# Optimization experiments

Hardware: AMD Instinct MI355X
Metric: run time of the kernel (lower is better)

The kernel has to match this reference:

```python
import jax, jax.numpy as jnp
import numpy as np

H = 64            # hidden_dim
N_NODES = 100000
N_EDGES = 2000000
IN_DIM = 2 * H + 2  # src_emb || dst_emb || src_fiedler || dst_fiedler


def setup_inputs() -> dict:
    key = jax.random.key(0)
    ks = jax.random.split(key, 10)
    node_embeddings = jax.random.normal(ks[0], (N_NODES, H), dtype=jnp.float32)
    edge_index = jax.random.randint(ks[1], (2, N_EDGES), 0, N_NODES, dtype=jnp.int64)
    fiedler_vector = jax.random.normal(ks[2], (N_NODES,), dtype=jnp.float32)
    # MLP scorer params: Linear(130,64)+ReLU, Linear(64,64)+ReLU, Linear(64,1)
    def lin(k, fan_in, fan_out):
        bound = 1.0 / np.sqrt(fan_in)
        kw, kb = jax.random.split(k)
        W = jax.random.uniform(kw, (fan_in, fan_out), jnp.float32, -bound, bound)
        b = jax.random.uniform(kb, (fan_out,), jnp.float32, -bound, bound)
        return W, b
    W1, b1 = lin(ks[3], IN_DIM, H)
    W2, b2 = lin(ks[4], H, H)
    W3, b3 = lin(ks[5], H, 1)
    return {
        "node_embeddings": node_embeddings,
        "fiedler_vector": fiedler_vector,
        "W1": W1, "b1": b1, "W2": W2, "b2": b2, "W3": W3, "b3": b3,
        "edge_index": edge_index,
        "num_nodes": N_NODES,
    }


def reference(node_embeddings, fiedler_vector, W1, b1, W2, b2, W3, b3, edge_index, num_nodes):
    src, dst = edge_index[0], edge_index[1]
    # Gather + concat edge features: [E, 2H+2]
    feats = jnp.concatenate(
        [
            node_embeddings[src],               # [E, H]
            node_embeddings[dst],               # [E, H]
            fiedler_vector[src][:, None],        # [E, 1]
            fiedler_vector[dst][:, None],        # [E, 1]
        ],
        axis=-1,
    )
    # Edge scorer MLP (Dropout is identity in eval mode)
    h = jax.nn.relu(feats @ W1 + b1)
    h = jax.nn.relu(h @ W2 + b2)
    edge_scores = (h @ W3 + b3)[:, 0]  # [E]
    return edge_scores
```

## Files before the change

### kernel.cpp

```cpp
#include <hip/hip_runtime.h>


#define HD 64

typedef __attribute__((ext_vector_type(8))) _Float16 half8;
typedef __attribute__((ext_vector_type(4))) _Float16 half4;
typedef __attribute__((ext_vector_type(8))) short  short8;
typedef __attribute__((ext_vector_type(8))) float  float8;
typedef __attribute__((ext_vector_type(4))) float  f32x4;

__device__ __forceinline__ half8 relu_h8(half8 x) {
    short8 b = __builtin_bit_cast(short8, x);
    short8 m = b >> 15;
    b = b & ~m;
    return __builtin_bit_cast(half8, b);
}

__global__ __launch_bounds__(256) void precompute_uv(
    const float* __restrict__ emb, const float* __restrict__ fied,
    const float* __restrict__ W1, const float* __restrict__ b1,
    _Float16* __restrict__ u, _Float16* __restrict__ v,
    int n_nodes, int ntiles)
{
    const int lane = threadIdx.x & 63;
    const int q = lane >> 4;
    const int c = lane & 15;
    const int wid = blockIdx.x * (blockDim.x >> 6) + (threadIdx.x >> 6);
    const int nw  = gridDim.x * (blockDim.x >> 6);

    half8 Au[4][2], Av[4][2];
    #pragma unroll
    for (int t = 0; t < 4; ++t)
        #pragma unroll
        for (int ks = 0; ks < 2; ++ks)
            #pragma unroll
            for (int j = 0; j < 8; ++j) {
                int k = ks * 32 + q * 8 + j;
                Au[t][ks][j] = (_Float16)W1[k * HD + t * 16 + c];
                Av[t][ks][j] = (_Float16)W1[(64 + k) * HD + t * 16 + c];
            }
    f32x4 b1q[4], wsq[4], wdq[4];
    #pragma unroll
    for (int t = 0; t < 4; ++t) {
        b1q[t] = *(const f32x4*)(b1 + t * 16 + q * 4);
        wsq[t] = *(const f32x4*)(W1 + 128 * HD + t * 16 + q * 4);
        wdq[t] = *(const f32x4*)(W1 + 129 * HD + t * 16 + q * 4);
    }

    for (int tile = wid; tile < ntiles; tile += nw) {
        const int n0 = tile * 16;
        const int n  = n0 + c;
        int na = n; if (na >= n_nodes) na = n_nodes - 1;
        const float* rp = emb + (size_t)na * HD + q * 8;
        float8 a0 = *(const float8*)rp;
        float8 a1 = *(const float8*)(rp + 32);
        half8 B0 = __builtin_convertvector(a0, half8);
        half8 B1 = __builtin_convertvector(a1, half8);

        f32x4 aU[4] = {}, aV[4] = {};
        #pragma unroll
        for (int t = 0; t < 4; ++t) {
            aU[t] = __builtin_amdgcn_mfma_f32_16x16x32_f16(Au[t][0], B0, aU[t], 0, 0, 0);
            aU[t] = __builtin_amdgcn_mfma_f32_16x16x32_f16(Au[t][1], B1, aU[t], 0, 0, 0);
            aV[t] = __builtin_amdgcn_mfma_f32_16x16x32_f16(Av[t][0], B0, aV[t], 0, 0, 0);
            aV[t] = __builtin_amdgcn_mfma_f32_16x16x32_f16(Av[t][1], B1, aV[t], 0, 0, 0);
        }

        const float fv = fied[na];
        const bool ok = (n < n_nodes);
        #pragma unroll
        for (int t = 0; t < 4; ++t) {
            half4 hu, hv;
            #pragma unroll
            for (int r = 0; r < 4; ++r) {
                hu[r] = (_Float16)(aU[t][r] + b1q[t][r] + fv * wsq[t][r]);
                hv[r] = (_Float16)(aV[t][r] + fv * wdq[t][r]);
            }
            if (ok) {
                *(half4*)(u + (size_t)n * HD + t * 16 + q * 4) = hu;
                *(half4*)(v + (size_t)n * HD + t * 16 + q * 4) = hv;
            }
        }
    }
}

__global__ __launch_bounds__(256) void edge_mlp(
    const _Float16* __restrict__ u, const _Float16* __restrict__ v,
    const int* __restrict__ src, const int* __restrict__ dst,
    const float* __restrict__ W2, const float* __restrict__ b2,
    const float* __restrict__ W3, const float* __restrict__ b3,
    float* __restrict__ out, int E, int ntiles)
{
    const int lane = threadIdx.x & 63;
    const int q = lane >> 4;
    const int c = lane & 15;
    const int wid = blockIdx.x * (blockDim.x >> 6) + (threadIdx.x >> 6);
    const int nw  = gridDim.x * (blockDim.x >> 6);

    half8 Af[4][2];
    #pragma unroll
    for (int t = 0; t < 4; ++t)
        #pragma unroll
        for (int ks = 0; ks < 2; ++ks)
            #pragma unroll
            for (int j = 0; j < 8; ++j) {
                int k = ks * 32 + q * 8 + j;
                Af[t][ks][j] = (_Float16)W2[k * HD + t * 16 + c];
            }
    f32x4 b2q[4], w3q[4];
    #pragma unroll
    for (int t = 0; t < 4; ++t) {
        b2q[t] = *(const f32x4*)(b2 + t * 16 + q * 4);
        w3q[t] = *(const f32x4*)(W3 + t * 16 + q * 4);
    }
    const float b3v = b3[0];

    const int stride = nw * 2;
    const int base0  = wid * 2;

    auto eid = [&](int tile) {
        int t = tile; if (t >= ntiles) t = ntiles - 1;
        int e = t * 16 + c; if (e >= E) e = E - 1;
        return e;
    };
    auto issue = [&](int s, int d, half8& Ua, half8& Ub, half8& Va, half8& Vb) {
        const half8* up = (const half8*)(u + (unsigned)s * HD + q * 8);
        const half8* vp = (const half8*)(v + (unsigned)d * HD + q * 8);
        Ua = up[0]; Ub = up[4]; Va = vp[0]; Vb = vp[4];
    };
    auto compute_store = [&](int tile, half8 Ua, half8 Ub, half8 Va, half8 Vb) {
        half8 B0 = relu_h8(Ua + Va);
        half8 B1 = relu_h8(Ub + Vb);
        f32x4 acc[4];
        #pragma unroll
        for (int t = 0; t < 4; ++t) acc[t] = b2q[t];
        #pragma unroll
        for (int t = 0; t < 4; ++t) {
            acc[t] = __builtin_amdgcn_mfma_f32_16x16x32_f16(Af[t][0], B0, acc[t], 0, 0, 0);
            acc[t] = __builtin_amdgcn_mfma_f32_16x16x32_f16(Af[t][1], B1, acc[t], 0, 0, 0);
        }
        float p = 0.f;
        #pragma unroll
        for (int t = 0; t < 4; ++t)
            #pragma unroll
            for (int r = 0; r < 4; ++r)
                p = fmaf(fmaxf(acc[t][r], 0.f), w3q[t][r], p);
        p += __shfl_xor(p, 16, 64);
        p += __shfl_xor(p, 32, 64);
        if (q == 0) {
            int e = tile * 16 + c;
            if (e < E) out[e] = p + b3v;
        }
    };

    if (base0 >= ntiles) return;

    int e0 = eid(base0), e1 = eid(base0 + 1);
    int s0 = src[e0], d0 = dst[e0];
    int s1 = src[e1], d1 = dst[e1];
    half8 U0a, U0b, V0a, V0b, U1a, U1b, V1a, V1b;
    issue(s0, d0, U0a, U0b, V0a, V0b);
    issue(s1, d1, U1a, U1b, V1a, V1b);
    int e2 = eid(base0 + stride), e3 = eid(base0 + stride + 1);
    int sc0 = src[e2], dc0 = dst[e2];
    int sc1 = src[e3], dc1 = dst[e3];

    for (int base = base0; base < ntiles; base += stride) {
        const int f0 = eid(base + 2 * stride), f1 = eid(base + 2 * stride + 1);
        const int sn0 = src[f0], dn0 = dst[f0];
        const int sn1 = src[f1], dn1 = dst[f1];

        compute_store(base, U0a, U0b, V0a, V0b);
        issue(sc0, dc0, U0a, U0b, V0a, V0b);

        compute_store(base + 1, U1a, U1b, V1a, V1b);
        issue(sc1, dc1, U1a, U1b, V1a, V1b);

        sc0 = sn0; dc0 = dn0; sc1 = sn1; dc1 = dn1;
    }
}

#define NCH 2048

__global__ __launch_bounds__(256) void hist_k(
    const int* __restrict__ src, const int* __restrict__ dst,
    unsigned* __restrict__ counts, int E, int CH, unsigned mul8)
{
    __shared__ unsigned h[64];
    const int b = blockIdx.x;
    for (int i = threadIdx.x; i < 64; i += 256) h[i] = 0u;
    __syncthreads();
    const int lo = b * CH;
    int hi = lo + CH; if (hi > E) hi = E;
    for (int i = lo + threadIdx.x; i < hi; i += 256) {
        unsigned s = (unsigned)src[i], d = (unsigned)dst[i];
        unsigned bk = __umulhi(s, mul8) * 8u + __umulhi(d, mul8);
        atomicAdd(&h[bk], 1u);
    }
    __syncthreads();
    for (int i = threadIdx.x; i < 64; i += 256) counts[(size_t)b * 64 + i] = h[i];
}

__global__ __launch_bounds__(256) void scanb_k(
    unsigned* __restrict__ counts, unsigned* __restrict__ totals)
{
    __shared__ unsigned part[256];
    const int bk = blockIdx.x;
    const int t  = threadIdx.x;
    unsigned vpre[8];
    unsigned sum = 0u;
    const int c0 = t * 8;
    #pragma unroll
    for (int j = 0; j < 8; ++j) {
        unsigned x = counts[(size_t)(c0 + j) * 64 + bk];
        vpre[j] = sum; sum += x;
    }
    part[t] = sum;
    __syncthreads();
    for (int d = 1; d < 256; d <<= 1) {
        unsigned x = (t >= d) ? part[t - d] : 0u;
        __syncthreads();
        part[t] += x;
        __syncthreads();
    }
    const unsigned incl = part[t];
    const unsigned excl = incl - sum;
    #pragma unroll
    for (int j = 0; j < 8; ++j)
        counts[(size_t)(c0 + j) * 64 + bk] = vpre[j] + excl;
    if (t == 255) totals[bk] = incl;
}

__global__ __launch_bounds__(64) void base_k(
    const unsigned* __restrict__ totals, unsigned* __restrict__ base)
{
    const int t = threadIdx.x;
    const unsigned own = totals[t];
    unsigned x = own;
    #pragma unroll
    for (int d = 1; d < 64; d <<= 1) {
        unsigned y = __shfl_up(x, d, 64);
        if (t >= d) x += y;
    }
    base[t] = x - own;
    if (t == 63) base[64] = x;
}

__global__ __launch_bounds__(256) void scat_k(
    const int* __restrict__ src, const int* __restrict__ dst,
    const unsigned* __restrict__ counts, const unsigned* __restrict__ base,
    unsigned long long* __restrict__ recs, int E, int CH, unsigned mul8)
{
    __shared__ unsigned cur[64];
    const int b = blockIdx.x;
    for (int i = threadIdx.x; i < 64; i += 256)
        cur[i] = base[i] + counts[(size_t)b * 64 + i];
    __syncthreads();
    const int lo = b * CH;
    int hi = lo + CH; if (hi > E) hi = E;
    for (int i = lo + threadIdx.x; i < hi; i += 256) {
        unsigned s = (unsigned)src[i], d = (unsigned)dst[i];
        unsigned bk = __umulhi(s, mul8) * 8u + __umulhi(d, mul8);
        unsigned slot = atomicAdd(&cur[bk], 1u);
        recs[slot] = (unsigned long long)s
                   | ((unsigned long long)d << 17)
                   | ((unsigned long long)(unsigned)i << 34);
    }
}

__global__ __launch_bounds__(256) void edge_mlp_b(
    const _Float16* __restrict__ u, const _Float16* __restrict__ v,
    const unsigned long long* __restrict__ recs,
    const unsigned* __restrict__ boff,
    const float* __restrict__ W2, const float* __restrict__ b2,
    const float* __restrict__ W3, const float* __restrict__ b3,
    float* __restrict__ out)
{
    const int lane = threadIdx.x & 63;
    const int q = lane >> 4;
    const int c = lane & 15;

    const int x   = blockIdx.x & 7;
    const int lb  = blockIdx.x >> 3;
    const int nlb = gridDim.x >> 3;

    const unsigned rs = boff[x * 8];
    const unsigned re = boff[x * 8 + 8];
    if (re <= rs) return;
    const int ntiles = (int)((re - rs + 15u) >> 4);

    half8 Af[4][2];
    #pragma unroll
    for (int t = 0; t < 4; ++t)
        #pragma unroll
        for (int ks = 0; ks < 2; ++ks)
            #pragma unroll
            for (int j = 0; j < 8; ++j) {
                int k = ks * 32 + q * 8 + j;
                Af[t][ks][j] = (_Float16)W2[k * HD + t * 16 + c];
            }
    f32x4 b2q[4], w3q[4];
    #pragma unroll
    for (int t = 0; t < 4; ++t) {
        b2q[t] = *(const f32x4*)(b2 + t * 16 + q * 4);
        w3q[t] = *(const f32x4*)(W3 + t * 16 + q * 4);
    }
    const float b3v = b3[0];

    const int wid = lb * ((int)blockDim.x >> 6) + (threadIdx.x >> 6);
    const int nw  = nlb * ((int)blockDim.x >> 6);
    const int stride = nw * 2;
    const int base0  = wid * 2;
    if (base0 >= ntiles) return;

    auto ridx = [&](int tile) -> unsigned {
        int t = tile; if (t >= ntiles) t = ntiles - 1;
        unsigned r = rs + (unsigned)t * 16u + (unsigned)c;
        if (r >= re) r = re - 1u;
        return r;
    };
    auto issue = [&](unsigned s, unsigned d, half8& Ua, half8& Ub, half8& Va, half8& Vb) {
        const half8* up = (const half8*)(u + (unsigned)s * HD + q * 8);
        const half8* vp = (const half8*)(v + (unsigned)d * HD + q * 8);
        Ua = up[0]; Ub = up[4]; Va = vp[0]; Vb = vp[4];
    };
    auto compute_store = [&](int tile, unsigned eid,
                             half8 Ua, half8 Ub, half8 Va, half8 Vb) {
        half8 B0 = relu_h8(Ua + Va);
        half8 B1 = relu_h8(Ub + Vb);
        f32x4 acc[4];
        #pragma unroll
        for (int t = 0; t < 4; ++t) acc[t] = b2q[t];
        #pragma unroll
        for (int t = 0; t < 4; ++t) {
            acc[t] = __builtin_amdgcn_mfma_f32_16x16x32_f16(Af[t][0], B0, acc[t], 0, 0, 0);
            acc[t] = __builtin_amdgcn_mfma_f32_16x16x32_f16(Af[t][1], B1, acc[t], 0, 0, 0);
        }
        float p = 0.f;
        #pragma unroll
        for (int t = 0; t < 4; ++t)
            #pragma unroll
            for (int r = 0; r < 4; ++r)
                p = fmaf(fmaxf(acc[t][r], 0.f), w3q[t][r], p);
        p += __shfl_xor(p, 16, 64);
        p += __shfl_xor(p, 32, 64);
        if (q == 0 && (rs + (unsigned)tile * 16u + (unsigned)c) < re)
            out[eid] = p + b3v;
    };

    unsigned long long r0 = recs[ridx(base0)];
    unsigned long long r1 = recs[ridx(base0 + 1)];
    unsigned e0 = (unsigned)(r0 >> 34);
    unsigned e1 = (unsigned)(r1 >> 34);
    half8 U0a, U0b, V0a, V0b, U1a, U1b, V1a, V1b;
    issue((unsigned)r0 & 0x1FFFFu, (unsigned)(r0 >> 17) & 0x1FFFFu, U0a, U0b, V0a, V0b);
    issue((unsigned)r1 & 0x1FFFFu, (unsigned)(r1 >> 17) & 0x1FFFFu, U1a, U1b, V1a, V1b);
    unsigned long long rc0 = recs[ridx(base0 + stride)];
    unsigned long long rc1 = recs[ridx(base0 + stride + 1)];

    for (int bse = base0; bse < ntiles; bse += stride) {
        const unsigned long long rn0 = recs[ridx(bse + 2 * stride)];
        const unsigned long long rn1 = recs[ridx(bse + 2 * stride + 1)];

        compute_store(bse, e0, U0a, U0b, V0a, V0b);
        e0 = (unsigned)(rc0 >> 34);
        issue((unsigned)rc0 & 0x1FFFFu, (unsigned)(rc0 >> 17) & 0x1FFFFu,
              U0a, U0b, V0a, V0b);

        compute_store(bse + 1, e1, U1a, U1b, V1a, V1b);
        e1 = (unsigned)(rc1 >> 34);
        issue((unsigned)rc1 & 0x1FFFFu, (unsigned)(rc1 >> 17) & 0x1FFFFu,
              U1a, U1b, V1a, V1b);

        rc0 = rn0; rc1 = rn1;
    }
}

extern "C" void kernel_launch(void* const* d_in, const int* in_sizes, int n_in,
                              void* d_out, int out_size, void* d_ws, size_t ws_size,
                              hipStream_t stream) {
    const float* emb  = (const float*)d_in[0];
    const float* fied = (const float*)d_in[1];
    const float* W1   = (const float*)d_in[2];
    const float* b1   = (const float*)d_in[3];
    const float* W2   = (const float*)d_in[4];
    const float* b2   = (const float*)d_in[5];
    const float* W3   = (const float*)d_in[6];
    const float* b3   = (const float*)d_in[7];
    const int*   eidx = (const int*)d_in[8];

    const int n_nodes = in_sizes[1];
    const int E       = in_sizes[8] / 2;
    const int* srcp = eidx;
    const int* dstp = eidx + E;

    _Float16* u = (_Float16*)d_ws;
    _Float16* v = u + (size_t)n_nodes * HD;
    const size_t uv_bytes = (size_t)n_nodes * HD * 2 * sizeof(_Float16);

    const int ntilesN = (n_nodes + 15) / 16;
    precompute_uv<<<1024, 256, 0, stream>>>(emb, fied, W1, b1, u, v,
                                            n_nodes, ntilesN);

    const size_t recs_off   = uv_bytes;
    const size_t counts_off = recs_off + (size_t)E * 8;
    const size_t totals_off = counts_off + (size_t)NCH * 64 * 4;
    const size_t base_off   = totals_off + 64 * 4;
    const size_t need       = base_off + 65 * 4;

    const bool can_bucket = (ws_size >= need) &&
                            (n_nodes <= 131072) && (n_nodes >= 4096) &&
                            ((long long)E < (1LL << 30));

    if (can_bucket) {
        unsigned long long* recs = (unsigned long long*)((char*)d_ws + recs_off);
        unsigned* counts = (unsigned*)((char*)d_ws + counts_off);
        unsigned* totals = (unsigned*)((char*)d_ws + totals_off);
        unsigned* basep  = (unsigned*)((char*)d_ws + base_off);
        const unsigned mul8 = (unsigned)((8ULL << 32) / (unsigned long long)n_nodes);
        const int CH = (E + NCH - 1) / NCH;

        hist_k <<<NCH, 256, 0, stream>>>(srcp, dstp, counts, E, CH, mul8);
        scanb_k<<<64,  256, 0, stream>>>(counts, totals);
        base_k <<<1,    64, 0, stream>>>(totals, basep);
        scat_k <<<NCH, 256, 0, stream>>>(srcp, dstp, counts, basep, recs, E, CH, mul8);
        edge_mlp_b<<<2048, 256, 0, stream>>>(u, v, recs, basep,
                                             W2, b2, W3, b3, (float*)d_out);
    } else {
        const int ntilesE = (E + 15) / 16;
        edge_mlp<<<2048, 256, 0, stream>>>(u, v, srcp, dstp, W2, b2, W3, b3,
                                           (float*)d_out, E, ntilesE);
    }
}
```

Measured before the change: 204.7 us.

## Bucket edges by fine source slice and stage source u rows in LDS

Edges are now bucketed into 256 source slices by 8 destination slices, where before it was 8 by 8. The histogram and scan kernels are reworked to handle 2048 buckets over 128 chunks. Each edge-MLP block loads its source slice of u (about 391 rows) into swizzled LDS and reads source embeddings from there, so only the v rows are gathered from global memory. This cuts global gather traffic but reduces the grid to 512 blocks of 512 threads with about 50KB of LDS each. That risks lower occupancy and load imbalance, since each source slice is handled by only two blocks.

```diff
diff --git a/kernel.cpp b/kernel.cpp
--- a/kernel.cpp
+++ b/kernel.cpp
@@ -2,6 +2,10 @@
 
 
 #define HD 64
+#define SRC_B 256
+#define DST_B 8
+#define NB (SRC_B * DST_B)
+#define NCH 128
 
 typedef __attribute__((ext_vector_type(8))) _Float16 half8;
 typedef __attribute__((ext_vector_type(4))) _Float16 half4;
@@ -180,87 +184,89 @@
     }
 }
 
-#define NCH 2048
 
 __global__ __launch_bounds__(256) void hist_k(
     const int* __restrict__ src, const int* __restrict__ dst,
-    unsigned* __restrict__ counts, int E, int CH, unsigned mul8)
-{
-    __shared__ unsigned h[64];
+    unsigned* __restrict__ counts, int E, int CH,
+    unsigned mulSL, unsigned mul8)
+{
+    __shared__ unsigned h[NB];
     const int b = blockIdx.x;
-    for (int i = threadIdx.x; i < 64; i += 256) h[i] = 0u;
+    for (int i = threadIdx.x; i < NB; i += 256) h[i] = 0u;
     __syncthreads();
     const int lo = b * CH;
     int hi = lo + CH; if (hi > E) hi = E;
     for (int i = lo + threadIdx.x; i < hi; i += 256) {
         unsigned s = (unsigned)src[i], d = (unsigned)dst[i];
-        unsigned bk = __umulhi(s, mul8) * 8u + __umulhi(d, mul8);
+        unsigned bk = __umulhi(s, mulSL) * 8u + __umulhi(d, mul8);
         atomicAdd(&h[bk], 1u);
     }
     __syncthreads();
-    for (int i = threadIdx.x; i < 64; i += 256) counts[(size_t)b * 64 + i] = h[i];
-}
-
-__global__ __launch_bounds__(256) void scanb_k(
+    for (int i = threadIdx.x; i < NB; i += 256)
+        counts[(size_t)b * NB + i] = h[i];
+}
+
+__global__ __launch_bounds__(NCH) void scanb_k(
     unsigned* __restrict__ counts, unsigned* __restrict__ totals)
 {
-    __shared__ unsigned part[256];
     const int bk = blockIdx.x;
     const int t  = threadIdx.x;
-    unsigned vpre[8];
-    unsigned sum = 0u;
-    const int c0 = t * 8;
-    #pragma unroll
-    for (int j = 0; j < 8; ++j) {
-        unsigned x = counts[(size_t)(c0 + j) * 64 + bk];
-        vpre[j] = sum; sum += x;
-    }
-    part[t] = sum;
-    __syncthreads();
-    for (int d = 1; d < 256; d <<= 1) {
-        unsigned x = (t >= d) ? part[t - d] : 0u;
-        __syncthreads();
-        part[t] += x;
-        __syncthreads();
-    }
-    const unsigned incl = part[t];
-    const unsigned excl = incl - sum;
-    #pragma unroll
-    for (int j = 0; j < 8; ++j)
-        counts[(size_t)(c0 + j) * 64 + bk] = vpre[j] + excl;
-    if (t == 255) totals[bk] = incl;
-}
-
-__global__ __launch_bounds__(64) void base_k(
+    unsigned x = counts[(size_t)t * NB + bk];
+    unsigned incl = x;
+    #pragma unroll
+    for (int d = 1; d < 64; d <<= 1) {
+        unsigned y = __shfl_up(incl, d, 64);
+        if ((t & 63) >= d) incl += y;
+    }
+    __shared__ unsigned wsum;
+    if (t == 63) wsum = incl;
+    __syncthreads();
+    if (t >= 64) incl += wsum;
+    counts[(size_t)t * NB + bk] = incl - x;
+    if (t == NCH - 1) totals[bk] = incl;
+}
+
+__global__ __launch_bounds__(1024) void base_k(
     const unsigned* __restrict__ totals, unsigned* __restrict__ base)
 {
     const int t = threadIdx.x;
-    const unsigned own = totals[t];
-    unsigned x = own;
+    const unsigned a = totals[2 * t];
+    const unsigned b = totals[2 * t + 1];
+    const unsigned s = a + b;
+    unsigned incl = s;
     #pragma unroll
     for (int d = 1; d < 64; d <<= 1) {
-        unsigned y = __shfl_up(x, d, 64);
-        if (t >= d) x += y;
-    }
-    base[t] = x - own;
-    if (t == 63) base[64] = x;
+        unsigned y = __shfl_up(incl, d, 64);
+        if ((t & 63) >= d) incl += y;
+    }
+    __shared__ unsigned wtot[16];
+    if ((t & 63) == 63) wtot[t >> 6] = incl;
+    __syncthreads();
+    unsigned woff = 0;
+    for (int w = 0; w < (t >> 6); ++w) woff += wtot[w];
+    incl += woff;
+    const unsigned excl = incl - s;
+    base[2 * t] = excl;
+    base[2 * t + 1] = excl + a;
+    if (t == 1023) base[NB] = incl;
 }
 
 __global__ __launch_bounds__(256) void scat_k(
     const int* __restrict__ src, const int* __restrict__ dst,
     const unsigned* __restrict__ counts, const unsigned* __restrict__ base,
-    unsigned long long* __restrict__ recs, int E, int CH, unsigned mul8)
-{
-    __shared__ unsigned cur[64];
+    unsigned long long* __restrict__ recs, int E, int CH,
+    unsigned mulSL, unsigned mul8)
+{
+    __shared__ unsigned cur[NB];
     const int b = blockIdx.x;
-    for (int i = threadIdx.x; i < 64; i += 256)
-        cur[i] = base[i] + counts[(size_t)b * 64 + i];
+    for (int i = threadIdx.x; i < NB; i += 256)
+        cur[i] = base[i] + counts[(size_t)b * NB + i];
     __syncthreads();
     const int lo = b * CH;
     int hi = lo + CH; if (hi > E) hi = E;
     for (int i = lo + threadIdx.x; i < hi; i += 256) {
         unsigned s = (unsigned)src[i], d = (unsigned)dst[i];
-        unsigned bk = __umulhi(s, mul8) * 8u + __umulhi(d, mul8);
+        unsigned bk = __umulhi(s, mulSL) * 8u + __umulhi(d, mul8);
         unsigned slot = atomicAdd(&cur[bk], 1u);
         recs[slot] = (unsigned long long)s
                    | ((unsigned long long)d << 17)
@@ -268,24 +274,33 @@
     }
 }
 
-__global__ __launch_bounds__(256) void edge_mlp_b(
+__global__ __launch_bounds__(512) void edge_mlp_l(
     const _Float16* __restrict__ u, const _Float16* __restrict__ v,
     const unsigned long long* __restrict__ recs,
-    const unsigned* __restrict__ boff,
+    const unsigned* __restrict__ base,
     const float* __restrict__ W2, const float* __restrict__ b2,
     const float* __restrict__ W3, const float* __restrict__ b3,
-    float* __restrict__ out)
-{
-    const int lane = threadIdx.x & 63;
+    float* __restrict__ out, int n_nodes, int SL)
+{
+    extern __shared__ _Float16 us[];
+    const int tid  = threadIdx.x;
+    const int lane = tid & 63;
     const int q = lane >> 4;
     const int c = lane & 15;
-
-    const int x   = blockIdx.x & 7;
-    const int lb  = blockIdx.x >> 3;
-    const int nlb = gridDim.x >> 3;
-
-    const unsigned rs = boff[x * 8];
-    const unsigned re = boff[x * 8 + 8];
+    const int sb = blockIdx.x >> 1;
+    const int hf = blockIdx.x & 1;
+
+    const int node0 = sb * SL;
+    int nrows = n_nodes - node0; if (nrows > SL) nrows = SL;
+    for (int i = tid; i < nrows * 8; i += 512) {
+        const int row = i >> 3, p = i & 7;
+        half8 val = *(const half8*)(u + (size_t)(node0 + row) * HD + p * 8);
+        *(half8*)(us + row * HD + ((p ^ (row & 7)) * 8)) = val;
+    }
+    __syncthreads();
+
+    const unsigned rs = base[sb * 8];
+    const unsigned re = base[sb * 8 + 8];
     if (re <= rs) return;
     const int ntiles = (int)((re - rs + 15u) >> 4);
 
@@ -307,10 +322,9 @@
     }
     const float b3v = b3[0];
 
-    const int wid = lb * ((int)blockDim.x >> 6) + (threadIdx.x >> 6);
-    const int nw  = nlb * ((int)blockDim.x >> 6);
-    const int stride = nw * 2;
-    const int base0  = wid * 2;
+    const int w = hf * 8 + (tid >> 6);
+    const int stride = 32;
+    const int base0  = w * 2;
     if (base0 >= ntiles) return;
 
     auto ridx = [&](int tile) -> unsigned {
@@ -319,13 +333,15 @@
         if (r >= re) r = re - 1u;
         return r;
     };
-    auto issue = [&](unsigned s, unsigned d, half8& Ua, half8& Ub, half8& Va, half8& Vb) {
-        const half8* up = (const half8*)(u + (unsigned)s * HD + q * 8);
+    auto issueV = [&](unsigned d, half8& Va, half8& Vb) {
         const half8* vp = (const half8*)(v + (unsigned)d * HD + q * 8);
-        Ua = up[0]; Ub = up[4]; Va = vp[0]; Vb = vp[4];
-    };
-    auto compute_store = [&](int tile, unsigned eid,
-                             half8 Ua, half8 Ub, half8 Va, half8 Vb) {
+        Va = vp[0]; Vb = vp[4];
+    };
+    auto compute_store = [&](int tile, unsigned eid, unsigned s,
+                             half8 Va, half8 Vb) {
+        const int sl = (int)s - node0;
+        const half8 Ua = *(const half8*)(us + sl * HD + ((q ^ (sl & 7)) * 8));
+        const half8 Ub = *(const half8*)(us + sl * HD + (((q + 4) ^ (sl & 7)) * 8));
         half8 B0 = relu_h8(Ua + Va);
         half8 B1 = relu_h8(Ub + Vb);
         f32x4 acc[4];
@@ -350,11 +366,12 @@
 
     unsigned long long r0 = recs[ridx(base0)];
     unsigned long long r1 = recs[ridx(base0 + 1)];
-    unsigned e0 = (unsigned)(r0 >> 34);
-    unsigned e1 = (unsigned)(r1 >> 34);
-    half8 U0a, U0b, V0a, V0b, U1a, U1b, V1a, V1b;
-    issue((unsigned)r0 & 0x1FFFFu, (unsigned)(r0 >> 17) & 0x1FFFFu, U0a, U0b, V0a, V0b);
-    issue((unsigned)r1 & 0x1FFFFu, (unsigned)(r1 >> 17) & 0x1FFFFu, U1a, U1b, V1a, V1b);
+    unsigned s0 = (unsigned)r0 & 0x1FFFFu, d0 = (unsigned)(r0 >> 17) & 0x1FFFFu;
+    unsigned s1 = (unsigned)r1 & 0x1FFFFu, d1 = (unsigned)(r1 >> 17) & 0x1FFFFu;
+    unsigned e0 = (unsigned)(r0 >> 34), e1 = (unsigned)(r1 >> 34);
+    half8 V0a, V0b, V1a, V1b;
+    issueV(d0, V0a, V0b);
+    issueV(d1, V1a, V1b);
     unsigned long long rc0 = recs[ridx(base0 + stride)];
     unsigned long long rc1 = recs[ridx(base0 + stride + 1)];
 
@@ -362,15 +379,15 @@
         const unsigned long long rn0 = recs[ridx(bse + 2 * stride)];
         const unsigned long long rn1 = recs[ridx(bse + 2 * stride + 1)];
 
-        compute_store(bse, e0, U0a, U0b, V0a, V0b);
+        compute_store(bse, e0, s0, V0a, V0b);
+        s0 = (unsigned)rc0 & 0x1FFFFu;
         e0 = (unsigned)(rc0 >> 34);
-        issue((unsigned)rc0 & 0x1FFFFu, (unsigned)(rc0 >> 17) & 0x1FFFFu,
-              U0a, U0b, V0a, V0b);
-
-        compute_store(bse + 1, e1, U1a, U1b, V1a, V1b);
+        issueV((unsigned)(rc0 >> 17) & 0x1FFFFu, V0a, V0b);
+
+        compute_store(bse + 1, e1, s1, V1a, V1b);
+        s1 = (unsigned)rc1 & 0x1FFFFu;
         e1 = (unsigned)(rc1 >> 34);
-        issue((unsigned)rc1 & 0x1FFFFu, (unsigned)(rc1 >> 17) & 0x1FFFFu,
-              U1a, U1b, V1a, V1b);
+        issueV((unsigned)(rc1 >> 17) & 0x1FFFFu, V1a, V1b);
 
         rc0 = rn0; rc1 = rn1;
     }
@@ -404,12 +421,16 @@
 
     const size_t recs_off   = uv_bytes;
     const size_t counts_off = recs_off + (size_t)E * 8;
-    const size_t totals_off = counts_off + (size_t)NCH * 64 * 4;
-    const size_t base_off   = totals_off + 64 * 4;
-    const size_t need       = base_off + 65 * 4;
+    const size_t totals_off = counts_off + (size_t)NCH * NB * 4;
+    const size_t base_off   = totals_off + (size_t)NB * 4;
+    const size_t need       = base_off + (size_t)(NB + 1) * 4;
+
+    const int SL = (n_nodes + SRC_B - 1) / SRC_B;
+    const size_t lds_bytes = (size_t)SL * HD * sizeof(_Float16);
 
     const bool can_bucket = (ws_size >= need) &&
                             (n_nodes <= 131072) && (n_nodes >= 4096) &&
+                            (lds_bytes <= 65536) &&
                             ((long long)E < (1LL << 30));
 
     if (can_bucket) {
@@ -417,15 +438,17 @@
         unsigned* counts = (unsigned*)((char*)d_ws + counts_off);
         unsigned* totals = (unsigned*)((char*)d_ws + totals_off);
         unsigned* basep  = (unsigned*)((char*)d_ws + base_off);
-        const unsigned mul8 = (unsigned)((8ULL << 32) / (unsigned long long)n_nodes);
+        const unsigned mulSL = (unsigned)(((1ULL << 32) + (unsigned)SL - 1) / (unsigned)SL);
+        const unsigned mul8  = (unsigned)((8ULL << 32) / (unsigned long long)n_nodes);
         const int CH = (E + NCH - 1) / NCH;
 
-        hist_k <<<NCH, 256, 0, stream>>>(srcp, dstp, counts, E, CH, mul8);
-        scanb_k<<<64,  256, 0, stream>>>(counts, totals);
-        base_k <<<1,    64, 0, stream>>>(totals, basep);
-        scat_k <<<NCH, 256, 0, stream>>>(srcp, dstp, counts, basep, recs, E, CH, mul8);
-        edge_mlp_b<<<2048, 256, 0, stream>>>(u, v, recs, basep,
-                                             W2, b2, W3, b3, (float*)d_out);
+        hist_k <<<NCH, 256, 0, stream>>>(srcp, dstp, counts, E, CH, mulSL, mul8);
+        scanb_k<<<NB,  NCH, 0, stream>>>(counts, totals);
+        base_k <<<1,  1024, 0, stream>>>(totals, basep);
+        scat_k <<<NCH, 256, 0, stream>>>(srcp, dstp, counts, basep, recs, E, CH,
+                                         mulSL, mul8);
+        edge_mlp_l<<<SRC_B * 2, 512, lds_bytes, stream>>>(
+            u, v, recs, basep, W2, b2, W3, b3, (float*)d_out, n_nodes, SL);
     } else {
         const int ntilesE = (E + 15) / 16;
         edge_mlp<<<2048, 256, 0, stream>>>(u, v, srcp, dstp, W2, b2, W3, b3,
```

Result: slower. 221.0 us (+7.9%).
